# Kernel tuning notes

Measured on AMD Instinct MI355X. Metric: run time of the kernel, lower is better.

## Reference

```python
import jax, jax.numpy as jnp
import numpy as np

N, E, IN, H, OUT = 100000, 1600000, 128, 128, 64


def setup_inputs() -> dict:
    key = jax.random.key(0)
    ks = jax.random.split(key, 6)
    glorot = lambda k, i, o: jax.random.normal(k, (i, o), jnp.float32) * np.float32(np.sqrt(2.0 / (i + o)))
    return dict(
        x=jax.random.normal(ks[0], (N, IN), jnp.float32),
        edge_index=jax.random.randint(ks[1], (2, E), 0, N, dtype=jnp.int64 if jax.config.jax_enable_x64 else jnp.int32),
        W1=glorot(ks[2], IN, H), b1=jnp.zeros((H,), jnp.float32),
        W2=glorot(ks[3], H, H), b2=jnp.zeros((H,), jnp.float32),
        W3=glorot(ks[4], H, OUT), b3=jnp.zeros((OUT,), jnp.float32),
    )


def _gcn_norm(edge_index, num_nodes):
    # add self loops with weight 1.0 (GCNConv add_self_loops=True, edge_weight=None -> ones)
    loop = jnp.arange(num_nodes, dtype=edge_index.dtype)
    src = jnp.concatenate([edge_index[0], loop])
    dst = jnp.concatenate([edge_index[1], loop])
    ew = jnp.ones(src.shape, jnp.float32)
    deg = jax.ops.segment_sum(ew, dst, num_segments=num_nodes)  # in-degree on dst
    dinv = jnp.where(deg > 0, jax.lax.rsqrt(deg), 0.0)
    norm = dinv[src] * ew * dinv[dst]  # [E+N]
    return src, dst, norm


def _conv(x, src, dst, norm, W, b):
    h = x @ W                                        # linear transform first (GCNConv order)
    msg = h[src] * norm[:, None]                     # gather + scale, [E+N, F]
    agg = jax.ops.segment_sum(msg, dst, num_segments=x.shape[0])  # scatter-add
    return agg + b


def reference(x, edge_index, W1, b1, W2, b2, W3, b3):
    # eval-mode forward: dropout is identity
    src, dst, norm = _gcn_norm(edge_index, x.shape[0])  # same graph -> norm shared across layers
    h = jax.nn.relu(_conv(x, src, dst, norm, W1, b1))
    h = jax.nn.relu(_conv(h, src, dst, norm, W2, b2))
    h = _conv(h, src, dst, norm, W3, b3)
    return jax.nn.log_softmax(h, axis=-1)
```

## Files before the change

### kernel.cpp

```cpp
#include <hip/hip_runtime.h>

typedef unsigned int u32;
typedef unsigned short u16;
typedef unsigned char u8;
typedef long i64;
typedef __attribute__((ext_vector_type(8))) short short8;
typedef __attribute__((ext_vector_type(4))) float f32x4;

#define MAXBIN 1024
#define SORT_TPB 1024
#define BINSLACK 2048

__device__ inline u16 f2bf(float f) {
    u32 u = __builtin_bit_cast(u32, f);
    u32 r = (u + 0x7fffu + ((u >> 16) & 1u)) >> 16;
    return (u16)r;
}

__device__ inline f32x4 mfma_fp8(uint2 a, uint2 b, f32x4 c) {
    return __builtin_amdgcn_mfma_f32_16x16x32_fp8_fp8(
        __builtin_bit_cast(i64, a), __builtin_bit_cast(i64, b), c, 0, 0, 0);
}

__device__ inline int permP(int p) {
    return ((p >> 5) << 5) + ((p & 3) << 3) + ((p >> 2) & 7);
}

__global__ __launch_bounds__(SORT_TPB) void k_bhist(const int* __restrict__ ei, int E, int W,
                                                    int* __restrict__ binTot, int NBIN) {
    __shared__ int h[MAXBIN];
    int tid = threadIdx.x;
    for (int i = tid; i < NBIN; i += SORT_TPB) h[i] = 0;
    __syncthreads();
    int s = blockIdx.x * W, e = min(E, s + W);
    for (int j = s + tid; j < e; j += SORT_TPB) atomicAdd(&h[ei[E + j] >> 7], 1);
    __syncthreads();
    for (int i = tid; i < NBIN; i += SORT_TPB) {
        int v = h[i];
        if (v) atomicAdd(&binTot[i], v);
    }
}

__global__ void k_bscan(const int* __restrict__ binTot, int NBIN,
                        int* __restrict__ binStart, int* __restrict__ binCur) {
    __shared__ int wsum[4];
    int t = threadIdx.x;
    int base = t * 4;
    int v0 = (base + 0 < NBIN) ? binTot[base + 0] : 0;
    int v1 = (base + 1 < NBIN) ? binTot[base + 1] : 0;
    int v2 = (base + 2 < NBIN) ? binTot[base + 2] : 0;
    int v3 = (base + 3 < NBIN) ? binTot[base + 3] : 0;
    int s = v0 + v1 + v2 + v3;
    int lane = t & 63, wv = t >> 6;
    int isc = s;
    for (int d = 1; d < 64; d <<= 1) { int o = __shfl_up(isc, d, 64); if (lane >= d) isc += o; }
    if (lane == 63) wsum[wv] = isc;
    __syncthreads();
    int woff = 0;
    for (int w = 0; w < wv; w++) woff += wsum[w];
    int run = woff + isc - s;
    if (base + 0 < NBIN) { binStart[base + 0] = run; binCur[base + 0] = run; } run += v0;
    if (base + 1 < NBIN) { binStart[base + 1] = run; binCur[base + 1] = run; } run += v1;
    if (base + 2 < NBIN) { binStart[base + 2] = run; binCur[base + 2] = run; } run += v2;
    if (base + 3 < NBIN) { binStart[base + 3] = run; binCur[base + 3] = run; }
    if (t == 255) binStart[NBIN] = wsum[0] + wsum[1] + wsum[2] + wsum[3];
}

__global__ __launch_bounds__(SORT_TPB) void k_bscatter(const int* __restrict__ ei, int E, int W,
                                                       int* __restrict__ binCur,
                                                       u32* __restrict__ binned, int NBIN) {
    __shared__ int lh[MAXBIN];
    __shared__ int lb[MAXBIN];
    int tid = threadIdx.x;
    for (int i = tid; i < NBIN; i += SORT_TPB) lh[i] = 0;
    __syncthreads();
    int s = blockIdx.x * W, e = min(E, s + W);
    for (int j = s + tid; j < e; j += SORT_TPB) atomicAdd(&lh[ei[E + j] >> 7], 1);
    __syncthreads();
    for (int i = tid; i < SORT_TPB ? 0 : 0; i++) {}
    for (int i = tid; i < NBIN; i += SORT_TPB) {
        int h = lh[i];
        lb[i] = h ? atomicAdd(&binCur[i], h) : 0;
    }
    __syncthreads();
    for (int i = tid; i < NBIN; i += SORT_TPB) lh[i] = 0;
    __syncthreads();
    for (int j = s + tid; j < e; j += SORT_TPB) {
        int d = ei[E + j];
        int b = d >> 7;
        int r = atomicAdd(&lh[b], 1);
        binned[lb[b] + r] = ((u32)ei[j] << 7) | (u32)(d & 127);
    }
}

__global__ __launch_bounds__(256) void k_bcsr(const u32* __restrict__ binned,
                                              const int* __restrict__ binStart,
                                              int N, int E, int* __restrict__ offs,
                                              int* __restrict__ ends,
                                              float* __restrict__ dinv,
                                              int* __restrict__ csr, int NBIN) {
    __shared__ int cnt[128];
    __shared__ int off[128];
    __shared__ int tot;
    int b = blockIdx.x;
    int tid = threadIdx.x;
    int dLo = b << 7;
    int nd = min(128, N - dLo);
    int e0 = binStart[b], e1 = binStart[b + 1];
    int pbase = e0 + b * BINSLACK;
    int pend = e1 + (b + 1) * BINSLACK;
    if (tid < 128) cnt[tid] = 0;
    __syncthreads();
    for (int j = e0 + tid; j < e1; j += 256) atomicAdd(&cnt[binned[j] & 127u], 1);
    __syncthreads();
    int c = (tid < 128) ? cnt[tid] : 0;
    int pc = (tid < 128) ? ((c + 16) & ~15) : 0;
    int lane = tid & 63;
    int isc = pc;
    for (int d = 1; d < 64; d <<= 1) { int o = __shfl_up(isc, d, 64); if (lane >= d) isc += o; }
    if (tid == 63) tot = isc;
    __syncthreads();
    int add = (tid >= 64 && tid < 128) ? tot : 0;
    if (tid < 128) off[tid] = add + isc - pc;
    for (int j = pbase + tid; j < pend; j += 256) csr[j] = N;
    __syncthreads();
    if (tid < nd) {
        offs[dLo + tid] = pbase + off[tid];
        ends[dLo + tid] = pbase + off[tid] + pc;
        dinv[dLo + tid] = rsqrtf((float)(c + 1));
        csr[pbase + off[tid] + c] = dLo + tid;
    }
    if (tid < 128) cnt[tid] = 0;
    __syncthreads();
    for (int j = e0 + tid; j < e1; j += 256) {
        u32 v = binned[j];
        int d7 = (int)(v & 127u);
        int r = atomicAdd(&cnt[d7], 1);
        csr[pbase + off[d7] + r] = (int)(v >> 7);
    }
}

__global__ void k_wtall(const float* __restrict__ W1, const float* __restrict__ W2,
                        const float* __restrict__ W3, u16* __restrict__ wt1,
                        u16* __restrict__ wt2, u16* __restrict__ wt3) {
    int idx = blockIdx.x * 256 + threadIdx.x;
    if (idx < 16384) {
        int k = idx >> 7, m = idx & 127;
        wt1[m * 128 + k] = f2bf(W1[idx]);
    } else if (idx < 32768) {
        int i = idx - 16384, p = i >> 7, m = i & 127;
        wt2[m * 128 + p] = f2bf(W2[permP(p) * 128 + m]);
    } else if (idx < 40960) {
        int i = idx - 32768, p = i >> 6, m = i & 63;
        wt3[m * 128 + p] = f2bf(W3[permP(p) * 64 + m]);
    }
}

template <int M, bool F32IN>
__global__ __launch_bounds__(256) void k_gemm(const void* __restrict__ xin,
                                              const u16* __restrict__ wt,
                                              const float* __restrict__ dinv,
                                              u8* __restrict__ g8, int N) {
    constexpr int K = 128;
    constexpr int LDK = 136;
    __shared__ u16 lwt[M * LDK];
    int tid = threadIdx.x;
    if (blockIdx.x == 0 && tid < M / 16)
        *(uint4*)(g8 + (size_t)N * M + (size_t)tid * 16) = make_uint4(0u, 0u, 0u, 0u);
    const uint4* wsrc = (const uint4*)wt;
#pragma unroll
    for (int c = tid; c < M * K / 8; c += 256) {
        int row = c >> 4, kc = c & 15;
        *(uint4*)&lwt[row * LDK + kc * 8] = wsrc[c];
    }
    __syncthreads();
    int lane = tid & 63, wv = tid >> 6;
    int node = blockIdx.x * 64 + wv * 16 + (lane & 15);
    int nodec = min(node, N - 1);
    int kr = (lane >> 4) * 8;
    f32x4 acc[M / 16];
#pragma unroll
    for (int t = 0; t < M / 16; t++) acc[t] = (f32x4){0.f, 0.f, 0.f, 0.f};
#pragma unroll
    for (int ks = 0; ks < 4; ks++) {
        short8 bfr;
        if (F32IN) {
            const float* xr = (const float*)xin + (size_t)nodec * K + ks * 32 + kr;
            float4 fa = *(const float4*)xr;
            float4 fb = *(const float4*)(xr + 4);
            bfr = (short8){(short)f2bf(fa.x), (short)f2bf(fa.y), (short)f2bf(fa.z),
                           (short)f2bf(fa.w), (short)f2bf(fb.x), (short)f2bf(fb.y),
                           (short)f2bf(fb.z), (short)f2bf(fb.w)};
        } else {
            bfr = *(const short8*)((const u16*)xin + (size_t)nodec * K + ks * 32 + kr);
        }
#pragma unroll
        for (int t = 0; t < M / 16; t++) {
            short8 afr = *(const short8*)&lwt[(t * 16 + (lane & 15)) * LDK + ks * 32 + kr];
            acc[t] = __builtin_amdgcn_mfma_f32_16x16x32_bf16(afr, bfr, acc[t], 0, 0, 0);
        }
    }
    if (node < N) {
        float dv16 = dinv[node] * 16.0f;
        int r0 = (lane >> 4) * 4;
#pragma unroll
        for (int t = 0; t < M / 16; t++) {
            u32 w = __builtin_amdgcn_cvt_pk_fp8_f32(acc[t][0] * dv16, acc[t][1] * dv16, 0, false);
            w = __builtin_amdgcn_cvt_pk_fp8_f32(acc[t][2] * dv16, acc[t][3] * dv16, w, true);
            *(u32*)(g8 + (size_t)node * M + t * 16 + r0) = w;
        }
    }
}

__global__ __launch_bounds__(256) void k_agg128(const u8* __restrict__ g8,
                                                const int* __restrict__ offs,
                                                const int* __restrict__ ends,
                                                const int* __restrict__ csr,
                                                const float* __restrict__ dinv,
                                                const float* __restrict__ bias,
                                                u16* __restrict__ hout, int N) {
    int wid = (blockIdx.x * 256 + threadIdx.x) >> 6;
    if (wid >= N) return;
    int lane = threadIdx.x & 63;
    int q = lane >> 4;
    int f = lane & 15;
    int s = offs[wid], e = ends[wid];
    uint2 bsel;
    bsel.x = (f < 4) ? (0x38u << (8 * f)) : 0u;
    bsel.y = (f >= 4 && f < 8) ? (0x38u << (8 * (f - 4))) : 0u;
    const u8* gf = g8 + f * 8;
    f32x4 ac0 = {0.f, 0.f, 0.f, 0.f}, ac1 = ac0, ac2 = ac0, ac3 = ac0;
    for (int j = s; j < e; j += 16) {
        int s0 = csr[j + q];
        int s1 = csr[j + 4 + q];
        int s2 = csr[j + 8 + q];
        int s3 = csr[j + 12 + q];
        uint2 w0 = *(const uint2*)(gf + ((u32)s0 << 7));
        uint2 w1 = *(const uint2*)(gf + ((u32)s1 << 7));
        uint2 w2 = *(const uint2*)(gf + ((u32)s2 << 7));
        uint2 w3 = *(const uint2*)(gf + ((u32)s3 << 7));
        ac0 = mfma_fp8(w0, bsel, ac0);
        ac1 = mfma_fp8(w1, bsel, ac1);
        ac2 = mfma_fp8(w2, bsel, ac2);
        ac3 = mfma_fp8(w3, bsel, ac3);
    }
    f32x4 a = (ac0 + ac1) + (ac2 + ac3);
    int jn = lane & 15, fq = lane >> 4;
    if (jn < 8) {
        float sc = dinv[wid] * 0.0625f;
        u32 o0, o1;
        {
            float v0 = fmaxf(fmaf(a[0], sc, bias[(4 * fq + 0) * 8 + jn]), 0.f);
            float v1 = fmaxf(fmaf(a[1], sc, bias[(4 * fq + 1) * 8 + jn]), 0.f);
            o0 = (u32)f2bf(v0) | ((u32)f2bf(v1) << 16);
        }
        {
            float v2 = fmaxf(fmaf(a[2], sc, bias[(4 * fq + 2) * 8 + jn]), 0.f);
            float v3 = fmaxf(fmaf(a[3], sc, bias[(4 * fq + 3) * 8 + jn]), 0.f);
            o1 = (u32)f2bf(v2) | ((u32)f2bf(v3) << 16);
        }
        *(uint2*)&hout[(size_t)wid * 128 + fq * 32 + jn * 4] = make_uint2(o0, o1);
    }
}

__global__ __launch_bounds__(256) void k_agg64(const u8* __restrict__ g8,
                                               const int* __restrict__ offs,
                                               const int* __restrict__ ends,
                                               const int* __restrict__ csr,
                                               const float* __restrict__ dinv,
                                               const float* __restrict__ bias,
                                               float* __restrict__ out, int N) {
    __shared__ float sm[4][64];
    int wid = (blockIdx.x * 256 + threadIdx.x) >> 6;
    if (wid >= N) return;
    int lane = threadIdx.x & 63;
    int wv = (int)(threadIdx.x >> 6);
    int q = lane >> 4;
    int f = lane & 15;
    int qq = q + ((f >> 3) << 2);
    int s = offs[wid], e = ends[wid];
    uint2 bsel;
    bsel.x = (f < 4) ? (0x38u << (8 * f)) : 0u;
    bsel.y = (f >= 4 && f < 8) ? (0x38u << (8 * (f - 4))) : 0u;
    const u8* gf = g8 + (f & 7) * 8;
    f32x4 ac0 = {0.f, 0.f, 0.f, 0.f}, ac1 = ac0;
    for (int j = s; j < e; j += 16) {
        int sA = csr[j + qq];
        int sB = csr[j + 8 + qq];
        uint2 wA = *(const uint2*)(gf + ((u32)sA << 6));
        uint2 wB = *(const uint2*)(gf + ((u32)sB << 6));
        ac0 = mfma_fp8(wA, bsel, ac0);
        ac1 = mfma_fp8(wB, bsel, ac1);
    }
    f32x4 a = ac0 + ac1;
#pragma unroll
    for (int r = 0; r < 4; r++) a[r] += __shfl_xor(a[r], 32, 64);
    int jn = lane & 15, fq = lane >> 4;
    bool act = (jn < 8) && (fq < 2);
    if (act) {
        float sc = dinv[wid] * 0.0625f;
        float v0 = fmaf(a[0], sc, bias[(4 * fq + 0) * 8 + jn]);
        float v1 = fmaf(a[1], sc, bias[(4 * fq + 1) * 8 + jn]);
        float v2 = fmaf(a[2], sc, bias[(4 * fq + 2) * 8 + jn]);
        float v3 = fmaf(a[3], sc, bias[(4 * fq + 3) * 8 + jn]);
        float m = fmaxf(fmaxf(v0, v1), fmaxf(v2, v3));
        m = fmaxf(m, __shfl_xor(m, 1, 64));
        m = fmaxf(m, __shfl_xor(m, 2, 64));
        m = fmaxf(m, __shfl_xor(m, 4, 64));
        m = fmaxf(m, __shfl_xor(m, 16, 64));
        float ss = __expf(v0 - m) + __expf(v1 - m) + __expf(v2 - m) + __expf(v3 - m);
        ss += __shfl_xor(ss, 1, 64);
        ss += __shfl_xor(ss, 2, 64);
        ss += __shfl_xor(ss, 4, 64);
        ss += __shfl_xor(ss, 16, 64);
        float lg = m + __logf(ss);
        sm[wv][(4 * fq + 0) * 8 + jn] = v0 - lg;
        sm[wv][(4 * fq + 1) * 8 + jn] = v1 - lg;
        sm[wv][(4 * fq + 2) * 8 + jn] = v2 - lg;
        sm[wv][(4 * fq + 3) * 8 + jn] = v3 - lg;
    }
    if (lane < 16) {
        float4 ov = *(float4*)&sm[wv][lane * 4];
        *(float4*)&out[(size_t)wid * 64 + lane * 4] = ov;
    }
}

extern "C" void kernel_launch(void* const* d_in, const int* in_sizes, int n_in,
                              void* d_out, int out_size, void* d_ws, size_t ws_size,
                              hipStream_t stream) {
    const float* x  = (const float*)d_in[0];
    const int*   ei = (const int*)d_in[1];
    const float* W1 = (const float*)d_in[2];
    const float* b1 = (const float*)d_in[3];
    const float* W2 = (const float*)d_in[4];
    const float* b2 = (const float*)d_in[5];
    const float* W3 = (const float*)d_in[6];
    const float* b3 = (const float*)d_in[7];
    const int N = in_sizes[0] / 128;
    const int E = in_sizes[1] / 2;
    const int NBIN = (N + 127) >> 7;

    char* ws = (char*)d_ws;
    size_t o = 0;
    auto alloc = [&](size_t bytes) -> char* {
        char* p = ws + o;
        o += (bytes + 255) & ~(size_t)255;
        return p;
    };
    int*   binTot = (int*)alloc((size_t)MAXBIN * 4);
    int*   binSt  = (int*)alloc((size_t)(MAXBIN + 1) * 4);
    int*   binCur = (int*)alloc((size_t)MAXBIN * 4);
    float* dinv   = (float*)alloc((size_t)N * 4);
    int*   offs   = (int*)alloc((size_t)N * 4);
    int*   endsA  = (int*)alloc((size_t)N * 4);
    int*   csr    = (int*)alloc(((size_t)E + (size_t)NBIN * BINSLACK + 64) * 4);
    u16*   wt1    = (u16*)alloc(128 * 128 * 2);
    u16*   wt2    = (u16*)alloc(128 * 128 * 2);
    u16*   wt3    = (u16*)alloc(64 * 128 * 2);
    u8*    g8     = (u8*)alloc(((size_t)N + 1) * 128);
    u16*   hbuf   = (u16*)alloc((size_t)N * 128 * 2);
    u32*   binned = (u32*)hbuf;
    float* outp   = (float*)d_out;

    hipMemsetAsync(binTot, 0, (size_t)MAXBIN * 4, stream);
    int W256 = (E + 255) / 256;
    k_bhist<<<256, SORT_TPB, 0, stream>>>(ei, E, W256, binTot, NBIN);
    k_bscan<<<1, 256, 0, stream>>>(binTot, NBIN, binSt, binCur);
    k_bscatter<<<256, SORT_TPB, 0, stream>>>(ei, E, W256, binCur, binned, NBIN);
    k_bcsr<<<NBIN, 256, 0, stream>>>(binned, binSt, N, E, offs, endsA, dinv, csr, NBIN);
    k_wtall<<<(40960 + 255) / 256, 256, 0, stream>>>(W1, W2, W3, wt1, wt2, wt3);

    int gG = (N + 63) / 64;
    int gA = (int)(((size_t)N * 64 + 255) / 256);

    k_gemm<128, true ><<<gG, 256, 0, stream>>>(x,    wt1, dinv, g8, N);
    k_agg128<<<gA, 256, 0, stream>>>(g8, offs, endsA, csr, dinv, b1, hbuf, N);
    k_gemm<128, false><<<gG, 256, 0, stream>>>(hbuf, wt2, dinv, g8, N);
    k_agg128<<<gA, 256, 0, stream>>>(g8, offs, endsA, csr, dinv, b2, hbuf, N);
    k_gemm<64,  false><<<gG, 256, 0, stream>>>(hbuf, wt3, dinv, g8, N);
    k_agg64<<<gA, 256, 0, stream>>>(g8, offs, endsA, csr, dinv, b3, outp, N);
}
```

Baseline: 309.8 us.

## Pad CSR rows to multiples of 8 and unroll gathers by 32 with masked tail

CSR row padding shrinks from multiples of 16 to multiples of 8, so fewer dummy entries are gathered per node (average degree is about 17). The aggregation loops in both kernels now take 32 edges per iteration with more loads in flight, and a predicated tail handles the remaining 8-edge chunks. The aim is to cut wasted gather bandwidth and raise memory-level parallelism. The cost is more registers and branchy tail code, which may lower occupancy.

```diff
diff --git a/kernel.cpp b/kernel.cpp
--- a/kernel.cpp
+++ b/kernel.cpp
@@ -77,7 +77,6 @@
     int s = blockIdx.x * W, e = min(E, s + W);
     for (int j = s + tid; j < e; j += SORT_TPB) atomicAdd(&lh[ei[E + j] >> 7], 1);
     __syncthreads();
-    for (int i = tid; i < SORT_TPB ? 0 : 0; i++) {}
     for (int i = tid; i < NBIN; i += SORT_TPB) {
         int h = lh[i];
         lb[i] = h ? atomicAdd(&binCur[i], h) : 0;
@@ -114,7 +113,7 @@
     for (int j = e0 + tid; j < e1; j += 256) atomicAdd(&cnt[binned[j] & 127u], 1);
     __syncthreads();
     int c = (tid < 128) ? cnt[tid] : 0;
-    int pc = (tid < 128) ? ((c + 16) & ~15) : 0;
+    int pc = (tid < 128) ? ((c + 8) & ~7) : 0;
     int lane = tid & 63;
     int isc = pc;
     for (int d = 1; d < 64; d <<= 1) { int o = __shfl_up(isc, d, 64); if (lane >= d) isc += o; }
@@ -230,20 +229,46 @@
     bsel.y = (f >= 4 && f < 8) ? (0x38u << (8 * (f - 4))) : 0u;
     const u8* gf = g8 + f * 8;
     f32x4 ac0 = {0.f, 0.f, 0.f, 0.f}, ac1 = ac0, ac2 = ac0, ac3 = ac0;
-    for (int j = s; j < e; j += 16) {
-        int s0 = csr[j + q];
-        int s1 = csr[j + 4 + q];
-        int s2 = csr[j + 8 + q];
-        int s3 = csr[j + 12 + q];
-        uint2 w0 = *(const uint2*)(gf + ((u32)s0 << 7));
-        uint2 w1 = *(const uint2*)(gf + ((u32)s1 << 7));
-        uint2 w2 = *(const uint2*)(gf + ((u32)s2 << 7));
-        uint2 w3 = *(const uint2*)(gf + ((u32)s3 << 7));
-        ac0 = mfma_fp8(w0, bsel, ac0);
-        ac1 = mfma_fp8(w1, bsel, ac1);
-        ac2 = mfma_fp8(w2, bsel, ac2);
-        ac3 = mfma_fp8(w3, bsel, ac3);
-    }
+    int j = s;
+    for (; e - j > 32; j += 32) {
+        int i0 = csr[j + q],      i1 = csr[j + 4 + q];
+        int i2 = csr[j + 8 + q],  i3 = csr[j + 12 + q];
+        int i4 = csr[j + 16 + q], i5 = csr[j + 20 + q];
+        int i6 = csr[j + 24 + q], i7 = csr[j + 28 + q];
+        uint2 g0 = *(const uint2*)(gf + ((u32)i0 << 7));
+        uint2 g1 = *(const uint2*)(gf + ((u32)i1 << 7));
+        uint2 g2 = *(const uint2*)(gf + ((u32)i2 << 7));
+        uint2 g3 = *(const uint2*)(gf + ((u32)i3 << 7));
+        uint2 g4 = *(const uint2*)(gf + ((u32)i4 << 7));
+        uint2 g5 = *(const uint2*)(gf + ((u32)i5 << 7));
+        uint2 g6 = *(const uint2*)(gf + ((u32)i6 << 7));
+        uint2 g7 = *(const uint2*)(gf + ((u32)i7 << 7));
+        ac0 = mfma_fp8(g0, bsel, ac0);
+        ac1 = mfma_fp8(g1, bsel, ac1);
+        ac2 = mfma_fp8(g2, bsel, ac2);
+        ac3 = mfma_fp8(g3, bsel, ac3);
+        ac0 = mfma_fp8(g4, bsel, ac0);
+        ac1 = mfma_fp8(g5, bsel, ac1);
+        ac2 = mfma_fp8(g6, bsel, ac2);
+        ac3 = mfma_fp8(g7, bsel, ac3);
+    }
+    int mu = (e - j) >> 3;
+    int i0 = csr[j + q], i1 = csr[j + 4 + q];
+    int i2 = 0, i3 = 0, i4 = 0, i5 = 0, i6 = 0, i7 = 0;
+    if (mu > 1) { i2 = csr[j + 8 + q];  i3 = csr[j + 12 + q]; }
+    if (mu > 2) { i4 = csr[j + 16 + q]; i5 = csr[j + 20 + q]; }
+    if (mu > 3) { i6 = csr[j + 24 + q]; i7 = csr[j + 28 + q]; }
+    uint2 g0 = *(const uint2*)(gf + ((u32)i0 << 7));
+    uint2 g1 = *(const uint2*)(gf + ((u32)i1 << 7));
+    uint2 g2 = make_uint2(0u, 0u), g3 = g2, g4 = g2, g5 = g2, g6 = g2, g7 = g2;
+    if (mu > 1) { g2 = *(const uint2*)(gf + ((u32)i2 << 7)); g3 = *(const uint2*)(gf + ((u32)i3 << 7)); }
+    if (mu > 2) { g4 = *(const uint2*)(gf + ((u32)i4 << 7)); g5 = *(const uint2*)(gf + ((u32)i5 << 7)); }
+    if (mu > 3) { g6 = *(const uint2*)(gf + ((u32)i6 << 7)); g7 = *(const uint2*)(gf + ((u32)i7 << 7)); }
+    ac0 = mfma_fp8(g0, bsel, ac0);
+    ac1 = mfma_fp8(g1, bsel, ac1);
+    if (mu > 1) { ac2 = mfma_fp8(g2, bsel, ac2); ac3 = mfma_fp8(g3, bsel, ac3); }
+    if (mu > 2) { ac0 = mfma_fp8(g4, bsel, ac0); ac1 = mfma_fp8(g5, bsel, ac1); }
+    if (mu > 3) { ac2 = mfma_fp8(g6, bsel, ac2); ac3 = mfma_fp8(g7, bsel, ac3); }
     f32x4 a = (ac0 + ac1) + (ac2 + ac3);
     int jn = lane & 15, fq = lane >> 4;
     if (jn < 8) {
@@ -283,16 +308,36 @@
     bsel.x = (f < 4) ? (0x38u << (8 * f)) : 0u;
     bsel.y = (f >= 4 && f < 8) ? (0x38u << (8 * (f - 4))) : 0u;
     const u8* gf = g8 + (f & 7) * 8;
-    f32x4 ac0 = {0.f, 0.f, 0.f, 0.f}, ac1 = ac0;
-    for (int j = s; j < e; j += 16) {
-        int sA = csr[j + qq];
-        int sB = csr[j + 8 + qq];
-        uint2 wA = *(const uint2*)(gf + ((u32)sA << 6));
-        uint2 wB = *(const uint2*)(gf + ((u32)sB << 6));
-        ac0 = mfma_fp8(wA, bsel, ac0);
-        ac1 = mfma_fp8(wB, bsel, ac1);
-    }
-    f32x4 a = ac0 + ac1;
+    f32x4 ac0 = {0.f, 0.f, 0.f, 0.f}, ac1 = ac0, ac2 = ac0, ac3 = ac0;
+    int j = s;
+    for (; e - j > 32; j += 32) {
+        int i0 = csr[j + qq], i1 = csr[j + 8 + qq];
+        int i2 = csr[j + 16 + qq], i3 = csr[j + 24 + qq];
+        uint2 g0 = *(const uint2*)(gf + ((u32)i0 << 6));
+        uint2 g1 = *(const uint2*)(gf + ((u32)i1 << 6));
+        uint2 g2 = *(const uint2*)(gf + ((u32)i2 << 6));
+        uint2 g3 = *(const uint2*)(gf + ((u32)i3 << 6));
+        ac0 = mfma_fp8(g0, bsel, ac0);
+        ac1 = mfma_fp8(g1, bsel, ac1);
+        ac2 = mfma_fp8(g2, bsel, ac2);
+        ac3 = mfma_fp8(g3, bsel, ac3);
+    }
+    int mu = (e - j) >> 3;
+    int i0 = csr[j + qq];
+    int i1 = 0, i2 = 0, i3 = 0;
+    if (mu > 1) i1 = csr[j + 8 + qq];
+    if (mu > 2) i2 = csr[j + 16 + qq];
+    if (mu > 3) i3 = csr[j + 24 + qq];
+    uint2 g0 = *(const uint2*)(gf + ((u32)i0 << 6));
+    uint2 g1 = make_uint2(0u, 0u), g2 = g1, g3 = g1;
+    if (mu > 1) g1 = *(const uint2*)(gf + ((u32)i1 << 6));
+    if (mu > 2) g2 = *(const uint2*)(gf + ((u32)i2 << 6));
+    if (mu > 3) g3 = *(const uint2*)(gf + ((u32)i3 << 6));
+    ac0 = mfma_fp8(g0, bsel, ac0);
+    if (mu > 1) ac1 = mfma_fp8(g1, bsel, ac1);
+    if (mu > 2) ac2 = mfma_fp8(g2, bsel, ac2);
+    if (mu > 3) ac3 = mfma_fp8(g3, bsel, ac3);
+    f32x4 a = (ac0 + ac1) + (ac2 + ac3);
 #pragma unroll
     for (int r = 0; r < 4; r++) a[r] += __shfl_xor(a[r], 32, 64);
     int jn = lane & 15, fq = lane >> 4;
```

Result: slower. 327.1 us (+5.6%).
